# Kernel optimization log

Measured on AMD Instinct MI355X. Metric: run time of the kernel, lower is better.

## Reference

```python
import jax, jax.numpy as jnp
import numpy as np
from jax import lax

N = 16384
K = 16
EPS = 1e-5


def setup_inputs() -> dict:
    key = jax.random.key(0)
    ks = jax.random.split(key, 10)

    def w(k, shape):
        fan_in = shape[0]
        return jax.random.normal(k, shape, jnp.float32) / np.sqrt(fan_in)

    return {
        "pos": jax.random.normal(ks[0], (N, 3), jnp.float32),
        "normal": jax.random.normal(ks[1], (N, 3), jnp.float32),
        # conv1 mlp: Linear(9,64) -> GroupNorm(8,64) -> ReLU -> Linear(64,64)
        "W1a": w(ks[2], (9, 64)), "b1a": jnp.zeros((64,), jnp.float32),
        "g1": jnp.ones((64,), jnp.float32), "beta1": jnp.zeros((64,), jnp.float32),
        "W1b": w(ks[3], (64, 64)), "b1b": jnp.zeros((64,), jnp.float32),
        # conv2 mlp: Linear(67,64) -> GroupNorm(8,64) -> ReLU -> Linear(64,64)
        "W2a": w(ks[4], (67, 64)), "b2a": jnp.zeros((64,), jnp.float32),
        "g2": jnp.ones((64,), jnp.float32), "beta2": jnp.zeros((64,), jnp.float32),
        "W2b": w(ks[5], (64, 64)), "b2b": jnp.zeros((64,), jnp.float32),
        # conv3 mlp: Linear(67,128) -> GroupNorm(16,128) -> ReLU -> Linear(128,128)
        "W3a": w(ks[6], (67, 128)), "b3a": jnp.zeros((128,), jnp.float32),
        "g3": jnp.ones((128,), jnp.float32), "beta3": jnp.zeros((128,), jnp.float32),
        "W3b": w(ks[7], (128, 128)), "b3b": jnp.zeros((128,), jnp.float32),
    }


def knn_graph(pos, k):
    # [N,N] squared distances; loop=True -> self is included (distance 0).
    sq = jnp.sum(pos * pos, axis=1)
    d2 = sq[:, None] + sq[None, :] - 2.0 * (pos @ pos.T)
    _, nbr = lax.top_k(-d2, k)  # [N,k] neighbor (source) indices per target node
    return nbr


def group_norm(h, gamma, beta, groups):
    # h: [N,k,C]; normalize each group of channels per edge sample.
    n, k, c = h.shape
    hg = h.reshape(n, k, groups, c // groups)
    mu = hg.mean(axis=-1, keepdims=True)
    var = hg.var(axis=-1, keepdims=True)
    hg = (hg - mu) * lax.rsqrt(var + EPS)
    return hg.reshape(n, k, c) * gamma + beta


def pointnet_conv(x, pos, nbr, Wa, ba, gamma, beta, Wb, bb, groups):
    # message: concat(x_j, pos_j - pos_i), MLP per edge, max-aggregate over neighbors
    xj = x[nbr]                              # [N,k,C_in]
    rel = pos[nbr] - pos[:, None, :]         # [N,k,3]
    m = jnp.concatenate([xj, rel], axis=-1)  # [N,k,C_in+3]
    h = m @ Wa + ba
    h = jax.nn.relu(group_norm(h, gamma, beta, groups))
    h = h @ Wb + bb
    return jnp.max(h, axis=1)                # [N,C_out]


def reference(pos, normal, W1a, b1a, g1, beta1, W1b, b1b,
              W2a, b2a, g2, beta2, W2b, b2b,
              W3a, b3a, g3, beta3, W3b, b3b):
    nbr = knn_graph(pos, K)
    h = jnp.concatenate([pos, normal], axis=-1)  # [N,6]
    h1 = jax.nn.relu(pointnet_conv(h, pos, nbr, W1a, b1a, g1, beta1, W1b, b1b, 8))
    h2 = jax.nn.relu(pointnet_conv(h1, pos, nbr, W2a, b2a, g2, beta2, W2b, b2b, 8))
    h3 = jax.nn.relu(pointnet_conv(h2, pos, nbr, W3a, b3a, g3, beta3, W3b, b3b, 16))
    return (h1, h2, h3)
```

## Files before the change

kernel.cpp:

```cpp
#include <hip/hip_runtime.h>
#include <hip/hip_bf16.h>
#include <stdint.h>

typedef unsigned long long u64;
typedef unsigned int u32;
typedef __attribute__((ext_vector_type(8))) short bf16x8;
typedef __attribute__((ext_vector_type(8))) unsigned short u16x8;
typedef __attribute__((ext_vector_type(4))) float f32x4;

__device__ __forceinline__ float ldv(const void* p, size_t idx, int mode) {
  return mode ? __bfloat162float(((const __hip_bfloat16*)p)[idx])
              : ((const float*)p)[idx];
}
__device__ __forceinline__ void stv(void* p, size_t idx, int mode, float v) {
  if (mode) ((__hip_bfloat16*)p)[idx] = __float2bfloat16(v);
  else      ((float*)p)[idx] = v;
}
__device__ __forceinline__ unsigned short f2bfb(float f) {
  u32 u = __float_as_uint(f);
  u32 r = u + 0x7fffu + ((u >> 16) & 1u);
  return (unsigned short)(r >> 16);
}
__device__ __forceinline__ float bfb2f(unsigned short b) {
  return __uint_as_float((u32)b << 16);
}
__device__ __forceinline__ u64 shfl64(u64 v, int src) {
  int lo = __shfl((int)(u32)(v & 0xffffffffu), src, 64);
  int hi = __shfl((int)(u32)(v >> 32), src, 64);
  return ((u64)(u32)hi << 32) | (u32)lo;
}
__device__ __forceinline__ u64 shflxor64(u64 v, int m) {
  int lo = __shfl_xor((int)(u32)(v & 0xffffffffu), m, 64);
  int hi = __shfl_xor((int)(u32)(v >> 32), m, 64);
  return ((u64)(u32)hi << 32) | (u32)lo;
}
__device__ __forceinline__ u64 shfl64w16(u64 v, int src) {
  int lo = __shfl((int)(u32)(v & 0xffffffffu), src, 16);
  int hi = __shfl((int)(u32)(v >> 32), src, 16);
  return ((u64)(u32)hi << 32) | (u32)lo;
}

__device__ __forceinline__ u32 benc(float f) {
  u32 u = __float_as_uint(f);
  return (u & 0x80000000u) ? ~u : (u | 0x80000000u);
}
__device__ __forceinline__ float bdec(u32 k) {
  return (k & 0x80000000u) ? __uint_as_float(k ^ 0x80000000u)
                           : __uint_as_float(~k);
}

__global__ void PointNetSimple_61409442398998_kernel() {}

struct CvtEnt { const void* src; float* dst; int n; };
struct CvtArgs { CvtEnt e[12]; };
struct WEnt { const void* src; unsigned short* dst; int K, N, Kpad; };
struct WArgs { WEnt e[6]; };

__global__ void setup_kernel(const void* __restrict__ pos,
                             const void* __restrict__ nrm,
                             WArgs wa, CvtArgs ca,
                             int* __restrict__ flag,
                             float4* __restrict__ pos4,
                             float* __restrict__ h0, int n) {
  const unsigned short* u16p = (const unsigned short*)pos;
  int cnt = 0;
  for (int k = 0; k < 32; ++k) {
    int e = (u16p[k] >> 7) & 0xff;
    if (e >= 110 && e <= 140) cnt++;
  }
  const int mode = (cnt >= 26) ? 1 : 0;

  const int nprep = n >> 8;
  const int b = blockIdx.x;
  if (b < nprep) {
    int i = b * 256 + threadIdx.x;
    float x = ldv(pos, 3*(size_t)i+0, mode);
    float y = ldv(pos, 3*(size_t)i+1, mode);
    float z = ldv(pos, 3*(size_t)i+2, mode);
    pos4[i] = make_float4(x, y, z, x*x + y*y + z*z);
    h0[6*(size_t)i+0] = x; h0[6*(size_t)i+1] = y; h0[6*(size_t)i+2] = z;
    h0[6*(size_t)i+3] = ldv(nrm, 3*(size_t)i+0, mode);
    h0[6*(size_t)i+4] = ldv(nrm, 3*(size_t)i+1, mode);
    h0[6*(size_t)i+5] = ldv(nrm, 3*(size_t)i+2, mode);
    float bmn[3] = {x, y, z}, bmx[3] = {x, y, z};
#pragma unroll
    for (int m = 32; m; m >>= 1) {
#pragma unroll
      for (int k = 0; k < 3; ++k) {
        bmn[k] = fminf(bmn[k], __shfl_xor(bmn[k], m, 64));
        bmx[k] = fmaxf(bmx[k], __shfl_xor(bmx[k], m, 64));
      }
    }
    if ((threadIdx.x & 63) == 0) {
      u32* bb = (u32*)flag;
#pragma unroll
      for (int k = 0; k < 3; ++k) {
        atomicMin(&bb[4 + k], benc(bmn[k]));
        atomicMax(&bb[7 + k], benc(bmx[k]));
      }
    }
  } else {
    int r = b - nprep;
    if (r < 6) {
      WEnt ent = wa.e[r];
      for (int t = threadIdx.x; t < ent.N * ent.Kpad; t += blockDim.x) {
        int nn = t / ent.Kpad;
        int k  = t - nn * ent.Kpad;
        float v = (k < ent.K) ? ldv(ent.src, (size_t)k * ent.N + nn, mode) : 0.0f;
        ent.dst[t] = f2bfb(v);
      }
      if (r == 0 && threadIdx.x == 0) flag[0] = mode;
    } else {
      for (int t2 = 0; t2 < 12; ++t2) {
        CvtEnt ent = ca.e[t2];
        for (int t = threadIdx.x; t < ent.n; t += blockDim.x)
          ent.dst[t] = ldv(ent.src, t, mode);
      }
    }
  }
}

template<int CAP>
__device__ __forceinline__ void knn_flush(u64* __restrict__ wbuf, int& cnt,
                                          u64& val, u64& t15, float& th,
                                          int lane) {
  u64 cand = (lane < cnt) ? wbuf[lane] : ~0ull;
#pragma unroll
  for (int k = 2; k <= CAP; k <<= 1) {
#pragma unroll
    for (int j = k >> 1; j > 0; j >>= 1) {
      u64 other = shflxor64(cand, j);
      bool up    = ((lane & k) == 0) || (k == CAP);
      bool lower = ((lane & j) == 0);
      bool keepMin = (up == lower);
      u64 mn = cand < other ? cand : other;
      u64 mx = cand < other ? other : cand;
      cand = keepMin ? mn : mx;
    }
  }
  u64 rev = shfl64w16(cand, 15 - (lane & 15));
  u64 lo = val < rev ? val : rev;
#pragma unroll
  for (int j = 8; j > 0; j >>= 1) {
    u64 other = shflxor64(lo, j);
    bool lower = ((lane & j) == 0);
    u64 mn = lo < other ? lo : other;
    u64 mx = lo < other ? other : lo;
    lo = lower ? mn : mx;
  }
  val = (lane < 16) ? lo : ~0ull;
  t15 = shfl64(val, 15);
  u32 thb = (u32)(t15 >> 32);
  th = (thb == 0xffffffffu) ? 3.4e38f : __uint_as_float(thb);
  cnt = 0;
}

#define GR 32
#define GR3 (GR*GR*GR)

__global__ __launch_bounds__(256) void hist_kernel(
    const float4* __restrict__ pos4, const u32* __restrict__ bbx,
    int* __restrict__ counts, int* __restrict__ cid, int n) {
  const int i = blockIdx.x * 256 + threadIdx.x;
  if (i >= n) return;
  const float mnx = bdec(bbx[0]), mny = bdec(bbx[1]), mnz = bdec(bbx[2]);
  const float ihx = (float)GR / fmaxf(bdec(bbx[3]) - mnx, 1e-20f);
  const float ihy = (float)GR / fmaxf(bdec(bbx[4]) - mny, 1e-20f);
  const float ihz = (float)GR / fmaxf(bdec(bbx[5]) - mnz, 1e-20f);
  float4 p = pos4[i];
  int cx = min(GR - 1, max(0, (int)((p.x - mnx) * ihx)));
  int cy = min(GR - 1, max(0, (int)((p.y - mny) * ihy)));
  int cz = min(GR - 1, max(0, (int)((p.z - mnz) * ihz)));
  int lin = (cz * GR + cy) * GR + cx;
  cid[i] = lin;
  atomicAdd(&counts[lin], 1);
}

__global__ __launch_bounds__(1024) void scan_kernel(
    const int* __restrict__ counts, int* __restrict__ cellstart,
    int* __restrict__ cursor) {
  __shared__ int part[1024];
  const int t = threadIdx.x;
  const int base = t * 32;
  int v[32];
  int s = 0;
#pragma unroll
  for (int k = 0; k < 32; ++k) { v[k] = counts[base + k]; s += v[k]; }
  part[t] = s;
  __syncthreads();
  for (int d = 1; d < 1024; d <<= 1) {
    int x = (t >= d) ? part[t - d] : 0;
    __syncthreads();
    part[t] += x;
    __syncthreads();
  }
  int off = part[t] - s;
#pragma unroll
  for (int k = 0; k < 32; ++k) {
    cellstart[base + k] = off; cursor[base + k] = off; off += v[k];
  }
  if (t == 1023) { cellstart[GR3] = off; cursor[GR3] = off; }
}

__global__ __launch_bounds__(256) void scatter_kernel(
    const float4* __restrict__ pos4, const int* __restrict__ cid,
    int* __restrict__ cursor, int* __restrict__ sidx,
    float4* __restrict__ spos4, int n) {
  const int i = blockIdx.x * 256 + threadIdx.x;
  if (i >= n) return;
  int dst = atomicAdd(&cursor[cid[i]], 1);
  spos4[dst] = pos4[i];
  sidx[dst]  = i;
}

#define KNN7_WPB 4
__global__ __launch_bounds__(256) void knn7_kernel(
    const float4* __restrict__ spos4,
    const int* __restrict__ sidx, const int* __restrict__ cellstart,
    const u32* __restrict__ bbx, int* __restrict__ nbr, int n) {
  __shared__ u64 buf[KNN7_WPB][72];
  const int tid = threadIdx.x, lane = tid & 63, w = tid >> 6;
  const int g = blockIdx.x * KNN7_WPB + w;
  u64* wbuf = &buf[w][0];
  const float4 pi = spos4[g];
  const int target = sidx[g];

  const float mnx = bdec(bbx[0]), mny = bdec(bbx[1]), mnz = bdec(bbx[2]);
  const float ex = fmaxf(bdec(bbx[3]) - mnx, 1e-20f);
  const float ey = fmaxf(bdec(bbx[4]) - mny, 1e-20f);
  const float ez = fmaxf(bdec(bbx[5]) - mnz, 1e-20f);
  const float ihx = (float)GR / ex, ihy = (float)GR / ey, ihz = (float)GR / ez;
  const float hxf = ex * (1.0f / GR), hyf = ey * (1.0f / GR), hzf = ez * (1.0f / GR);
  const int cx = min(GR - 1, max(0, (int)((pi.x - mnx) * ihx)));
  const int cy = min(GR - 1, max(0, (int)((pi.y - mny) * ihy)));
  const int cz = min(GR - 1, max(0, (int)((pi.z - mnz) * ihz)));

  u64 val = ~0ull, t15 = ~0ull;
  float th = 3.4e38f;
  int cnt = 0;
  int myseen = 0;

  auto doFlush = [&]() {
    if (cnt <= 32) knn_flush<32>(wbuf, cnt, val, t15, th, lane);
    else           knn_flush<64>(wbuf, cnt, val, t15, th, lane);
  };

  auto procSeg = [&](int p0, int p1) {
#pragma unroll 2
    for (int t0 = p0; t0 < p1; t0 += 64) {
      int gi = t0 + lane;
      bool in = gi < p1;
      float4 a = spos4[in ? gi : (p1 - 1)];
      float d2 = (pi.w + a.w) - 2.0f*(pi.x*a.x + pi.y*a.y + pi.z*a.z);
      d2 = fmaxf(d2, 0.0f);
      bool pass = in && (d2 <= th);
      u64 bal = __ballot(pass);
      if (bal) {
        int pc = __popcll(bal);
        if (cnt + pc > 64) doFlush();
        u32 mb = __builtin_amdgcn_mbcnt_lo((u32)bal, 0u);
        mb = __builtin_amdgcn_mbcnt_hi((u32)(bal >> 32), mb);
        if (pass)
          wbuf[cnt + mb] = ((u64)__float_as_uint(d2) << 32) | (u32)sidx[gi];
        cnt += pc;
      }
    }
  };

  {
    const int oc = (cz * GR + cy) * GR + cx;
    const int oLo = cellstart[oc], oHi = cellstart[oc + 1];
    if (lane == 0) myseen += oHi - oLo;
    procSeg(oLo, oHi);
    if (cnt > 0) doFlush();
  }

  for (int r = 1; r < GR; ++r) {
    const int x0 = max(cx - r, 0), x1 = min(cx + r, GR - 1);
    const int d1 = 2*r + 1, d2i = 2*r - 1;
    const int nA = 2 * d1;
    const int nB = 2 * d2i;
    const int nC = 2 * d2i * d2i;
    const int S = nA + nB + nC;
    const u32 magic = 0xFFFFFFFFu / (u32)d2i + 1u;

    for (int b0 = 0; b0 < S; b0 += 64) {
      const int s = b0 + lane;
      int zc = 0, yc = 0, xa = 0, xb = -1;
      bool live = s < S;
      if (live) {
        if (s < nA) {
          int za = s >= d1;
          int dy = s - (za ? d1 : 0) - r;
          zc = cz + (za ? r : -r); yc = cy + dy; xa = x0; xb = x1;
        } else if (s < nA + nB) {
          int t = s - nA;
          int side = t >= d2i;
          int dz = t - (side ? d2i : 0) - (r - 1);
          zc = cz + dz; yc = cy + (side ? r : -r); xa = x0; xb = x1;
        } else {
          int t = s - nA - nB;
          int side = t & 1; t >>= 1;
          int dzi = (int)__umulhi((u32)t, magic);
          int dyi = t - dzi * d2i;
          zc = cz - r + 1 + dzi; yc = cy - r + 1 + dyi;
          int xcell = side ? cx + r : cx - r;
          xa = xcell; xb = xcell;
          live = ((unsigned)xcell < GR);
        }
        live = live && ((unsigned)zc < GR) && ((unsigned)yc < GR);
      }
      int lo = 0, hi = 0;
      if (live) {
        int base = (zc * GR + yc) * GR;
        lo = cellstart[base + xa];
        hi = cellstart[base + xb + 1];
        myseen += hi - lo;
      }
      u64 bal = __ballot(live && (hi > lo));
      while (bal) {
        int l = __builtin_ctzll(bal); bal &= bal - 1;
        int p0 = __shfl(lo, l, 64), p1 = __shfl(hi, l, 64);
        procSeg(p0, p1);
      }
    }
    if (cnt > 0) doFlush();

    int tot = myseen;
#pragma unroll
    for (int m = 32; m; m >>= 1) tot += __shfl_xor(tot, m, 64);
    if (tot >= n) break;
    float mind = 3.4e38f;
    if (cx - r > 0)      mind = fminf(mind, pi.x - (mnx + (float)(cx - r) * hxf));
    if (cx + r < GR - 1) mind = fminf(mind, (mnx + (float)(cx + r + 1) * hxf) - pi.x);
    if (cy - r > 0)      mind = fminf(mind, pi.y - (mny + (float)(cy - r) * hyf));
    if (cy + r < GR - 1) mind = fminf(mind, (mny + (float)(cy + r + 1) * hyf) - pi.y);
    if (cz - r > 0)      mind = fminf(mind, pi.z - (mnz + (float)(cz - r) * hzf));
    if (cz + r < GR - 1) mind = fminf(mind, (mnz + (float)(cz + r + 1) * hzf) - pi.z);
    float mind2 = mind * mind * 0.9999f - 1e-6f;
    if (mind2 > th) break;
  }
  if (cnt > 0) doFlush();
  if (lane < 16) nbr[(size_t)target * 16 + lane] = (int)(val & 0xffffffffu);
}

template<int CIN, int CMID, int KT1, int NT, int KT2>
__global__ __launch_bounds__(256, 4) void conv_mfma6_kernel(
    const float* __restrict__ xf,
    const unsigned short* __restrict__ xb,
    const float4* __restrict__ pos4,
    const int* __restrict__ nbr,
    const int* __restrict__ flag,
    const unsigned short* __restrict__ WaT,
    const unsigned short* __restrict__ WbT,
    const float* __restrict__ baf,
    const float* __restrict__ gmf,
    const float* __restrict__ btf,
    const float* __restrict__ bbf,
    unsigned short* __restrict__ xoutb,
    void* __restrict__ bout, size_t out_off)
{
  constexpr int K1PAD = KT1 * 32;
  constexpr int SB = CMID + 8;

  __shared__ unsigned short msgB[128 * SB];

  const int tid  = threadIdx.x;
  const int lane = tid & 63;
  const int w    = tid >> 6;
  const int quad = lane >> 4;
  const int cl   = lane & 15;
  const int node0 = blockIdx.x * 8;
  const int mode = flag[0];

  bf16x8 afr[2][KT1];
#pragma unroll
  for (int mt = 0; mt < 2; ++mt) {
    const int node = node0 + w*2 + mt;
    const int j = nbr[(size_t)node*16 + cl];
    const float4 pin = pos4[node];
    const float4 pj = pos4[j];
    const float rx = pj.x - pin.x, ry = pj.y - pin.y, rz = pj.z - pin.z;
    if constexpr (CIN == 64) {
#pragma unroll
      for (int kt = 0; kt < 2; ++kt)
        afr[mt][kt] = *(const bf16x8*)&xb[(size_t)j*64 + kt*32 + quad*8];
      unsigned short o[8] = {0,0,0,0,0,0,0,0};
      if (quad == 0) { o[0] = f2bfb(rx); o[1] = f2bfb(ry); o[2] = f2bfb(rz); }
      afr[mt][KT1-1] = *(bf16x8*)o;
    } else {
      unsigned short o[8] = {0,0,0,0,0,0,0,0};
      if (quad == 0) {
        const float* p = &xf[(size_t)j*6];
        o[0] = f2bfb(p[0]); o[1] = f2bfb(p[1]); o[2] = f2bfb(p[2]);
        o[3] = f2bfb(p[3]); o[4] = f2bfb(p[4]); o[5] = f2bfb(p[5]);
        o[6] = f2bfb(rx);   o[7] = f2bfb(ry);
      } else if (quad == 1) {
        o[0] = f2bfb(rz);
      }
      afr[mt][0] = *(bf16x8*)o;
    }
  }

  const int grow = lane >> 1, ggl = lane & 1;
#pragma unroll
  for (int nt = 0; nt < NT; ++nt) {
    f32x4 a1[2];
    a1[0] = (f32x4){0.f, 0.f, 0.f, 0.f};
    a1[1] = (f32x4){0.f, 0.f, 0.f, 0.f};
#pragma unroll
    for (int kt = 0; kt < KT1; ++kt) {
      bf16x8 bfr = *(const bf16x8*)&WaT[(size_t)(nt*16 + cl) * K1PAD + kt*32 + quad*8];
      a1[0] = __builtin_amdgcn_mfma_f32_16x16x32_bf16(afr[0][kt], bfr, a1[0], 0, 0, 0);
      a1[1] = __builtin_amdgcn_mfma_f32_16x16x32_bf16(afr[1][kt], bfr, a1[1], 0, 0, 0);
    }
    float bac = baf[nt*16 + cl];
#pragma unroll
    for (int mt = 0; mt < 2; ++mt)
#pragma unroll
      for (int reg = 0; reg < 4; ++reg)
        msgB[(w*32 + mt*16 + quad*4 + reg) * SB + nt*16 + cl] =
            f2bfb(a1[mt][reg] + bac);
    asm volatile("" ::: "memory");
    {
      const int cb = nt*16 + ggl*8;
      unsigned short* p = &msgB[(w*32 + grow) * SB + cb];
      u16x8 hv = *(const u16x8*)p;
      float vv[8];
#pragma unroll
      for (int e = 0; e < 8; ++e) vv[e] = bfb2f(hv[e]);
      float s = 0.f, q = 0.f;
#pragma unroll
      for (int e = 0; e < 8; ++e) { s += vv[e]; q += vv[e]*vv[e]; }
      float mu = s * 0.125f;
      float var = q * 0.125f - mu * mu;
      float inv = rsqrtf(fmaxf(var, 0.0f) + 1e-5f);
      unsigned short o[8];
#pragma unroll
      for (int e = 0; e < 8; ++e) {
        float t = (vv[e] - mu) * inv * gmf[cb+e] + btf[cb+e];
        o[e] = f2bfb(fmaxf(t, 0.0f));
      }
      *(bf16x8*)p = *(bf16x8*)o;
    }
    asm volatile("" ::: "memory");
  }

  f32x4 acc2[2][NT];
#pragma unroll
  for (int mt = 0; mt < 2; ++mt)
#pragma unroll
    for (int nt = 0; nt < NT; ++nt) acc2[mt][nt] = (f32x4){0.f, 0.f, 0.f, 0.f};
#pragma unroll
  for (int kt = 0; kt < KT2; ++kt) {
    bf16x8 af0 = *(const bf16x8*)&msgB[(w*32 + cl)      * SB + kt*32 + quad*8];
    bf16x8 af1 = *(const bf16x8*)&msgB[(w*32 + 16 + cl) * SB + kt*32 + quad*8];
#pragma unroll
    for (int nt = 0; nt < NT; ++nt) {
      bf16x8 bfr = *(const bf16x8*)&WbT[(size_t)(nt*16 + cl) * CMID + kt*32 + quad*8];
      acc2[0][nt] = __builtin_amdgcn_mfma_f32_16x16x32_bf16(af0, bfr, acc2[0][nt], 0, 0, 0);
      acc2[1][nt] = __builtin_amdgcn_mfma_f32_16x16x32_bf16(af1, bfr, acc2[1][nt], 0, 0, 0);
    }
  }

#pragma unroll
  for (int mt = 0; mt < 2; ++mt) {
    int node = node0 + w*2 + mt;
#pragma unroll
    for (int nt = 0; nt < NT; ++nt) {
      float m = fmaxf(fmaxf(acc2[mt][nt][0], acc2[mt][nt][1]),
                      fmaxf(acc2[mt][nt][2], acc2[mt][nt][3]));
      m = fmaxf(m, __shfl_xor(m, 16, 64));
      m = fmaxf(m, __shfl_xor(m, 32, 64));
      float v = fmaxf(m + bbf[nt*16 + cl], 0.0f);
      if (quad == 0) {
        size_t oi = (size_t)node * CMID + nt*16 + cl;
        if (xoutb) xoutb[oi] = f2bfb(v);
        stv(bout, out_off + oi, mode, v);
      }
    }
  }
}

extern "C" void kernel_launch(void* const* d_in, const int* in_sizes, int n_in,
                              void* d_out, int out_size, void* d_ws, size_t ws_size,
                              hipStream_t stream) {
  (void)n_in; (void)ws_size; (void)in_sizes;
  int n = out_size / 256;
  if (n <= 0 || (n & 255)) n = 16384;

  float* ws = (float*)d_ws;
  int*    flag    = (int*)ws;
  float4* pos4    = (float4*)(ws + 16);
  float*  h0      = ws + 16 + (size_t)4*n;
  int*    nbr     = (int*)(ws + 16 + (size_t)10*n);
  unsigned short* h1b = (unsigned short*)(ws + 16 + (size_t)26*n);
  unsigned short* h2b = (unsigned short*)(ws + 16 + (size_t)58*n);
  float*  vbuf    = ws + 16 + (size_t)90*n;
  unsigned short* wtbuf = (unsigned short*)(vbuf + 1024);

  float* gbase = vbuf + 1024 + 22528;
  int*    cid       = (int*)gbase;
  int*    counts    = cid + n;
  int*    cellstart = counts + GR3;
  int*    cursor    = cellstart + 32772;
  int*    sidx      = cursor + 32772;
  float4* spos4     = (float4*)(sidx + n);

  const int vsz[12] = {64,64,64,64, 64,64,64,64, 128,128,128,128};
  const int vsrc[12] = {3,4,5,7, 9,10,11,13, 15,16,17,19};
  CvtArgs ca;
  float* vptr[12];
  {
    int off = 0;
    for (int t = 0; t < 12; ++t) {
      ca.e[t].src = d_in[vsrc[t]];
      ca.e[t].dst = vbuf + off;
      ca.e[t].n   = vsz[t];
      vptr[t] = vbuf + off;
      off += vsz[t];
    }
  }
  const int wK[6]    = {9, 64, 67, 64, 67, 128};
  const int wN[6]    = {64, 64, 64, 64, 128, 128};
  const int wKp[6]   = {32, 64, 96, 64, 96, 128};
  const int wsrc[6]  = {2, 6, 8, 12, 14, 18};
  WArgs wa;
  unsigned short* wptr[6];
  {
    int off = 0;
    for (int t = 0; t < 6; ++t) {
      wa.e[t].src  = d_in[wsrc[t]];
      wa.e[t].dst  = wtbuf + off;
      wa.e[t].K    = wK[t];
      wa.e[t].N    = wN[t];
      wa.e[t].Kpad = wKp[t];
      wptr[t] = wtbuf + off;
      off += wN[t] * wKp[t];
    }
  }

  u32* bbx = (u32*)ws + 4;
  hipMemsetAsync(bbx,     0xFF, 12, stream);
  hipMemsetAsync(bbx + 3, 0x00, 12, stream);
  hipMemsetAsync(counts,  0x00, GR3 * sizeof(int), stream);

  setup_kernel<<<n/256 + 7, 256, 0, stream>>>(
      d_in[0], d_in[1], wa, ca, flag, pos4, h0, n);

  hist_kernel<<<n/256, 256, 0, stream>>>(pos4, bbx, counts, cid, n);
  scan_kernel<<<1, 1024, 0, stream>>>(counts, cellstart, cursor);
  scatter_kernel<<<n/256, 256, 0, stream>>>(pos4, cid, cursor, sidx, spos4, n);
  knn7_kernel<<<n/KNN7_WPB, 256, 0, stream>>>(spos4, sidx, cellstart,
                                              bbx, nbr, n);

  conv_mfma6_kernel<6, 64, 1, 4, 2><<<n/8, 256, 0, stream>>>(
      h0, (const unsigned short*)nullptr, pos4, nbr, flag, wptr[0], wptr[1],
      vptr[0], vptr[1], vptr[2], vptr[3], h1b, d_out, (size_t)0);
  conv_mfma6_kernel<64, 64, 3, 4, 2><<<n/8, 256, 0, stream>>>(
      (const float*)nullptr, h1b, pos4, nbr, flag, wptr[2], wptr[3],
      vptr[4], vptr[5], vptr[6], vptr[7], h2b, d_out, (size_t)n*64);
  conv_mfma6_kernel<64, 128, 3, 8, 4><<<n/8, 256, 0, stream>>>(
      (const float*)nullptr, h2b, pos4, nbr, flag, wptr[4], wptr[5],
      vptr[8], vptr[9], vptr[10], vptr[11],
      (unsigned short*)nullptr, d_out, (size_t)n*128);
}
```

Before: 361.0 us.

## Replace bitonic-merge KNN flush with threshold-select compaction and final sort

The KNN kernel's per-flush bitonic sort and merge into a running top-16 is replaced by a larger 128-entry candidate buffer. When that buffer fills, it is compacted with a ballot-based binary search for a distance threshold that keeps at least 16 candidates. Only one full 64-wide bitonic sort runs at the end. Blocks grow to 8 waves of 512 threads. The aim is to cut shuffle-heavy sorting during the search, at the cost of looser thresholds that may let more candidates pass and repeated ballot loops.

After: 390.7 us. 8.2% more time.

```diff
diff --git a/kernel.cpp b/kernel.cpp
--- a/kernel.cpp
+++ b/kernel.cpp
@@ -24,21 +24,11 @@
 __device__ __forceinline__ float bfb2f(unsigned short b) {
   return __uint_as_float((u32)b << 16);
 }
-__device__ __forceinline__ u64 shfl64(u64 v, int src) {
-  int lo = __shfl((int)(u32)(v & 0xffffffffu), src, 64);
-  int hi = __shfl((int)(u32)(v >> 32), src, 64);
-  return ((u64)(u32)hi << 32) | (u32)lo;
-}
 __device__ __forceinline__ u64 shflxor64(u64 v, int m) {
   int lo = __shfl_xor((int)(u32)(v & 0xffffffffu), m, 64);
   int hi = __shfl_xor((int)(u32)(v >> 32), m, 64);
   return ((u64)(u32)hi << 32) | (u32)lo;
 }
-__device__ __forceinline__ u64 shfl64w16(u64 v, int src) {
-  int lo = __shfl((int)(u32)(v & 0xffffffffu), src, 16);
-  int hi = __shfl((int)(u32)(v >> 32), src, 16);
-  return ((u64)(u32)hi << 32) | (u32)lo;
-}
 
 __device__ __forceinline__ u32 benc(float f) {
   u32 u = __float_as_uint(f);
@@ -47,6 +37,23 @@
 __device__ __forceinline__ float bdec(u32 k) {
   return (k & 0x80000000u) ? __uint_as_float(k ^ 0x80000000u)
                            : __uint_as_float(~k);
+}
+
+__device__ __forceinline__ u64 sort64(u64 cand, int lane) {
+#pragma unroll
+  for (int k = 2; k <= 64; k <<= 1) {
+#pragma unroll
+    for (int j = k >> 1; j > 0; j >>= 1) {
+      u64 other = shflxor64(cand, j);
+      bool up    = ((lane & k) == 0) || (k == 64);
+      bool lower = ((lane & j) == 0);
+      bool keepMin = (up == lower);
+      u64 mn = cand < other ? cand : other;
+      u64 mx = cand < other ? other : cand;
+      cand = keepMin ? mn : mx;
+    }
+  }
+  return cand;
 }
 
 __global__ void PointNetSimple_61409442398998_kernel() {}
@@ -118,41 +125,6 @@
       }
     }
   }
-}
-
-template<int CAP>
-__device__ __forceinline__ void knn_flush(u64* __restrict__ wbuf, int& cnt,
-                                          u64& val, u64& t15, float& th,
-                                          int lane) {
-  u64 cand = (lane < cnt) ? wbuf[lane] : ~0ull;
-#pragma unroll
-  for (int k = 2; k <= CAP; k <<= 1) {
-#pragma unroll
-    for (int j = k >> 1; j > 0; j >>= 1) {
-      u64 other = shflxor64(cand, j);
-      bool up    = ((lane & k) == 0) || (k == CAP);
-      bool lower = ((lane & j) == 0);
-      bool keepMin = (up == lower);
-      u64 mn = cand < other ? cand : other;
-      u64 mx = cand < other ? other : cand;
-      cand = keepMin ? mn : mx;
-    }
-  }
-  u64 rev = shfl64w16(cand, 15 - (lane & 15));
-  u64 lo = val < rev ? val : rev;
-#pragma unroll
-  for (int j = 8; j > 0; j >>= 1) {
-    u64 other = shflxor64(lo, j);
-    bool lower = ((lane & j) == 0);
-    u64 mn = lo < other ? lo : other;
-    u64 mx = lo < other ? other : lo;
-    lo = lower ? mn : mx;
-  }
-  val = (lane < 16) ? lo : ~0ull;
-  t15 = shfl64(val, 15);
-  u32 thb = (u32)(t15 >> 32);
-  th = (thb == 0xffffffffu) ? 3.4e38f : __uint_as_float(thb);
-  cnt = 0;
 }
 
 #define GR 32
@@ -213,14 +185,16 @@
   sidx[dst]  = i;
 }
 
-#define KNN7_WPB 4
-__global__ __launch_bounds__(256) void knn7_kernel(
+#define KNN8_WPB 8
+#define KCAP 128
+
+__global__ __launch_bounds__(512) void knn8_kernel(
     const float4* __restrict__ spos4,
     const int* __restrict__ sidx, const int* __restrict__ cellstart,
     const u32* __restrict__ bbx, int* __restrict__ nbr, int n) {
-  __shared__ u64 buf[KNN7_WPB][72];
+  __shared__ u64 buf[KNN8_WPB][KCAP];
   const int tid = threadIdx.x, lane = tid & 63, w = tid >> 6;
-  const int g = blockIdx.x * KNN7_WPB + w;
+  const int g = blockIdx.x * KNN8_WPB + w;
   u64* wbuf = &buf[w][0];
   const float4 pi = spos4[g];
   const int target = sidx[g];
@@ -235,14 +209,59 @@
   const int cy = min(GR - 1, max(0, (int)((pi.y - mny) * ihy)));
   const int cz = min(GR - 1, max(0, (int)((pi.z - mnz) * ihz)));
 
-  u64 val = ~0ull, t15 = ~0ull;
+  u64 TH = ~0ull;
   float th = 3.4e38f;
   int cnt = 0;
+  bool tight = false;
   int myseen = 0;
 
-  auto doFlush = [&]() {
-    if (cnt <= 32) knn_flush<32>(wbuf, cnt, val, t15, th, lane);
-    else           knn_flush<64>(wbuf, cnt, val, t15, th, lane);
+  auto compact = [&](int TARGET) {
+    u64 k0 = wbuf[lane];
+    u64 k1 = wbuf[64 + lane];
+    const bool v0 = lane < cnt, v1 = (64 + lane) < cnt;
+    const u32 d0 = (u32)(k0 >> 32), d1 = (u32)(k1 >> 32);
+    u32 mn = min(v0 ? d0 : 0xffffffffu, v1 ? d1 : 0xffffffffu);
+    u32 mx = max(v0 ? d0 : 0u, v1 ? d1 : 0u);
+#pragma unroll
+    for (int m = 32; m; m >>= 1) {
+      mn = min(mn, (u32)__shfl_xor((int)mn, m, 64));
+      mx = max(mx, (u32)__shfl_xor((int)mx, m, 64));
+    }
+    u32 lo32 = mn, hi32 = mx;
+    int cb = cnt;
+    while (cb > TARGET && lo32 < hi32) {
+      u32 mid = lo32 + ((hi32 - lo32) >> 1);
+      int c = __popcll(__ballot(v0 && d0 <= mid)) +
+              __popcll(__ballot(v1 && d1 <= mid));
+      if (c >= 16) { hi32 = mid; cb = c; } else lo32 = mid + 1;
+    }
+    u64 THn = ((u64)hi32 << 32) | 0xffffffffull;
+    if (cb > 64) {
+      u64 l = (u64)hi32 << 32, h = THn;
+      while (cb > 64 && l < h) {
+        u64 mid = l + ((h - l) >> 1);
+        int c = __popcll(__ballot(v0 && k0 <= mid)) +
+                __popcll(__ballot(v1 && k1 <= mid));
+        if (c >= 16) { h = mid; cb = c; } else l = mid + 1;
+      }
+      THn = h;
+    }
+    TH = THn;
+    th = __uint_as_float((u32)(TH >> 32));
+    bool kp0 = v0 && k0 <= TH, kp1 = v1 && k1 <= TH;
+    u64 b0 = __ballot(kp0);
+    u32 p0 = __builtin_amdgcn_mbcnt_lo((u32)b0, 0u);
+    p0 = __builtin_amdgcn_mbcnt_hi((u32)(b0 >> 32), p0);
+    u64 b1 = __ballot(kp1);
+    u32 p1 = __builtin_amdgcn_mbcnt_lo((u32)b1, 0u);
+    p1 = __builtin_amdgcn_mbcnt_hi((u32)(b1 >> 32), p1);
+    int base1 = __popcll(b0);
+    asm volatile("" ::: "memory");
+    if (kp0) wbuf[p0] = k0;
+    if (kp1) wbuf[base1 + p1] = k1;
+    asm volatile("" ::: "memory");
+    cnt = base1 + __popcll(b1);
+    tight = true;
   };
 
   auto procSeg = [&](int p0, int p1) {
@@ -257,7 +276,7 @@
       u64 bal = __ballot(pass);
       if (bal) {
         int pc = __popcll(bal);
-        if (cnt + pc > 64) doFlush();
+        if (cnt + pc > KCAP) compact(32);
         u32 mb = __builtin_amdgcn_mbcnt_lo((u32)bal, 0u);
         mb = __builtin_amdgcn_mbcnt_hi((u32)(bal >> 32), mb);
         if (pass)
@@ -272,7 +291,7 @@
     const int oLo = cellstart[oc], oHi = cellstart[oc + 1];
     if (lane == 0) myseen += oHi - oLo;
     procSeg(oLo, oHi);
-    if (cnt > 0) doFlush();
+    if (cnt >= 16) compact(24);
   }
 
   for (int r = 1; r < GR; ++r) {
@@ -284,8 +303,8 @@
     const int S = nA + nB + nC;
     const u32 magic = 0xFFFFFFFFu / (u32)d2i + 1u;
 
-    for (int b0 = 0; b0 < S; b0 += 64) {
-      const int s = b0 + lane;
+    for (int b0i = 0; b0i < S; b0i += 64) {
+      const int s = b0i + lane;
       int zc = 0, yc = 0, xa = 0, xb = -1;
       bool live = s < S;
       if (live) {
@@ -324,7 +343,7 @@
         procSeg(p0, p1);
       }
     }
-    if (cnt > 0) doFlush();
+    if (cnt >= 16 && (!tight || cnt >= 48)) compact(24);
 
     int tot = myseen;
 #pragma unroll
@@ -340,8 +359,11 @@
     float mind2 = mind * mind * 0.9999f - 1e-6f;
     if (mind2 > th) break;
   }
-  if (cnt > 0) doFlush();
-  if (lane < 16) nbr[(size_t)target * 16 + lane] = (int)(val & 0xffffffffu);
+
+  if (cnt > 64) compact(32);
+  u64 cand = (lane < cnt) ? wbuf[lane] : ~0ull;
+  cand = sort64(cand, lane);
+  if (lane < 16) nbr[(size_t)target * 16 + lane] = (int)(cand & 0xffffffffu);
 }
 
 template<int CIN, int CMID, int KT1, int NT, int KT2>
@@ -551,7 +573,7 @@
   hist_kernel<<<n/256, 256, 0, stream>>>(pos4, bbx, counts, cid, n);
   scan_kernel<<<1, 1024, 0, stream>>>(counts, cellstart, cursor);
   scatter_kernel<<<n/256, 256, 0, stream>>>(pos4, cid, cursor, sidx, spos4, n);
-  knn7_kernel<<<n/KNN7_WPB, 256, 0, stream>>>(spos4, sidx, cellstart,
+  knn8_kernel<<<n/KNN8_WPB, 512, 0, stream>>>(spos4, sidx, cellstart,
                                               bbx, nbr, n);
 
   conv_mfma6_kernel<6, 64, 1, 4, 2><<<n/8, 256, 0, stream>>>(
```
